# Kernel tuning notes

Measured on AMD Instinct MI355X. Metric: run time of the kernel, lower is better.

Reference implementation:

```python
import jax, jax.numpy as jnp
import numpy as np

N = 8192      # reg_num == number of nodes
E = 524288    # number of edges
OUT = 32      # out_num


def gcn_conv(x, src, dst, W, b, n):
    """PyG GCNConv: add self-loops, symmetric deg^-1/2 normalization, linear, scatter-add, bias."""
    loop = jnp.arange(n)
    s = jnp.concatenate([src, loop])
    d = jnp.concatenate([dst, loop])
    deg = jax.ops.segment_sum(jnp.ones(s.shape, dtype=x.dtype), d, num_segments=n)
    dinv = jnp.where(deg > 0, jax.lax.rsqrt(deg), jnp.zeros_like(deg))
    norm = dinv[s] * dinv[d]                      # [E+N]
    h = x @ W.T                                    # [N, out_ch]
    out = jax.ops.segment_sum(norm[:, None] * h[s], d, num_segments=n)
    return out + b


def setup_inputs() -> dict:
    key = jax.random.key(0)
    ks = jax.random.split(key, 12)
    data = jax.random.normal(ks[0], (N, 2), dtype=jnp.float32)
    edge = jax.random.randint(ks[1], (2, E), 0, N, dtype=jnp.int64)
    # GCNConv weights (PyG Linear: y = x @ W.T, bias added after aggregation)
    W1 = jax.random.normal(ks[2], (4, 2), dtype=jnp.float32) * 0.5
    b1 = jnp.zeros((4,), dtype=jnp.float32)
    W2 = jax.random.normal(ks[3], (2, 4), dtype=jnp.float32) * 0.5
    b2 = jnp.zeros((2,), dtype=jnp.float32)
    W3 = jax.random.normal(ks[4], (1, 2), dtype=jnp.float32) * 0.5
    b3 = jnp.zeros((1,), dtype=jnp.float32)
    # trailing MLP: Linear(N, 2N) -> Tanh -> Linear(2N, OUT) -> Tanh
    Wa = jax.random.normal(ks[5], (2 * N, N), dtype=jnp.float32) * (1.0 / np.sqrt(N))
    ba = jnp.zeros((2 * N,), dtype=jnp.float32)
    Wb = jax.random.normal(ks[6], (OUT, 2 * N), dtype=jnp.float32) * (1.0 / np.sqrt(2 * N))
    bb = jnp.zeros((OUT,), dtype=jnp.float32)
    return {"data": data, "edge": edge, "W1": W1, "b1": b1, "W2": W2, "b2": b2,
            "W3": W3, "b3": b3, "Wa": Wa, "ba": ba, "Wb": Wb, "bb": bb}


def reference(data, edge, W1, b1, W2, b2, W3, b3, Wa, ba, Wb, bb):
    src, dst = edge[0], edge[1]
    n = data.shape[0]
    out = jax.nn.relu(gcn_conv(data, src, dst, W1, b1, n))
    out = jax.nn.relu(gcn_conv(out, src, dst, W2, b2, n))
    out = gcn_conv(out, src, dst, W3, b3, n)       # [N, 1]
    out = out.reshape(1, -1)                        # [1, N]
    out = jnp.tanh(out @ Wa.T + ba)                 # [1, 2N]
    out = jnp.tanh(out @ Wb.T + bb)                 # [1, OUT]
    return out
```

## Files before the change

kernel.cpp:

```cpp
#include <hip/hip_runtime.h>
#include <hip/hip_bf16.h>

#define NN   8192
#define NE   524288
#define DH   16384
#define NOUT 32

typedef float f32x4 __attribute__((ext_vector_type(4)));


__global__ __launch_bounds__(256) void k_hist(const int* __restrict__ dst, int* cnt) {
    int e = blockIdx.x * blockDim.x + threadIdx.x;
    if (e < NE) atomicAdd(&cnt[dst[e]], 1);
}

__global__ __launch_bounds__(256) void k_scan(const int* __restrict__ cnt,
                                              int* __restrict__ row,
                                              int* __restrict__ cursor,
                                              float* __restrict__ dinv) {
    __shared__ int sm[256];
    int t = threadIdx.x;
    int base = t * 32;
    int local[32];
    int sum = 0;
#pragma unroll
    for (int k = 0; k < 32; ++k) { local[k] = cnt[base + k]; sum += local[k]; }
    sm[t] = sum;
    __syncthreads();
    for (int off = 1; off < 256; off <<= 1) {
        int v = (t >= off) ? sm[t - off] : 0;
        __syncthreads();
        sm[t] += v;
        __syncthreads();
    }
    int pre = (t == 0) ? 0 : sm[t - 1];
#pragma unroll
    for (int k = 0; k < 32; ++k) {
        row[base + k] = pre;
        cursor[base + k] = pre;
        dinv[base + k] = rsqrtf((float)local[k] + 1.0f);
        pre += local[k];
    }
    if (t == 255) row[NN] = pre;
}

__global__ __launch_bounds__(256) void k_build(const int* __restrict__ src,
                                               const int* __restrict__ dst,
                                               int* __restrict__ cursor,
                                               int* __restrict__ srcs) {
    int e = blockIdx.x * blockDim.x + threadIdx.x;
    if (e >= NE) return;
    int p = atomicAdd(&cursor[dst[e]], 1);
    srcs[p] = src[e];
}

__global__ __launch_bounds__(256) void k_h1(const float* __restrict__ x0,
                                            const float* __restrict__ W1,
                                            float* __restrict__ h1) {
    int i = blockIdx.x * blockDim.x + threadIdx.x;
    if (i >= NN) return;
    float a = x0[2 * i], b = x0[2 * i + 1];
    f32x4 h;
#pragma unroll
    for (int c = 0; c < 4; ++c) h[c] = a * W1[2 * c] + b * W1[2 * c + 1];
    *(f32x4*)(h1 + 4 * i) = h;
}


__global__ __launch_bounds__(256) void k_g4(const int* __restrict__ row,
                                            const int* __restrict__ srcs,
                                            const float* __restrict__ dinv,
                                            const float* __restrict__ h1,
                                            const float* __restrict__ b1,
                                            const float* __restrict__ W2,
                                            float* __restrict__ h2) {
    int wid = threadIdx.x >> 6, lane = threadIdx.x & 63;
    int i = blockIdx.x * 4 + wid;
    int beg = row[i], end = row[i + 1];
    float a0 = 0, a1 = 0, a2 = 0, a3 = 0;
    for (int p = beg + lane; p < end; p += 64) {
        int s = srcs[p];
        float w = dinv[s];
        float4 hv = *(const float4*)(h1 + 4 * s);
        a0 += w * hv.x; a1 += w * hv.y; a2 += w * hv.z; a3 += w * hv.w;
    }
#pragma unroll
    for (int off = 32; off > 0; off >>= 1) {
        a0 += __shfl_down(a0, off, 64);
        a1 += __shfl_down(a1, off, 64);
        a2 += __shfl_down(a2, off, 64);
        a3 += __shfl_down(a3, off, 64);
    }
    if (lane == 0) {
        float di = dinv[i];
        float4 hs = *(const float4*)(h1 + 4 * i);
        float x0v = fmaxf(di * (a0 + di * hs.x) + b1[0], 0.0f);
        float x1v = fmaxf(di * (a1 + di * hs.y) + b1[1], 0.0f);
        float x2v = fmaxf(di * (a2 + di * hs.z) + b1[2], 0.0f);
        float x3v = fmaxf(di * (a3 + di * hs.w) + b1[3], 0.0f);
        float2 o;
        o.x = x0v * W2[0] + x1v * W2[1] + x2v * W2[2] + x3v * W2[3];
        o.y = x0v * W2[4] + x1v * W2[5] + x2v * W2[6] + x3v * W2[7];
        *(float2*)(h2 + 2 * i) = o;
    }
}

__global__ __launch_bounds__(256) void k_g2(const int* __restrict__ row,
                                            const int* __restrict__ srcs,
                                            const float* __restrict__ dinv,
                                            const float* __restrict__ h2,
                                            const float* __restrict__ b2,
                                            const float* __restrict__ W3,
                                            float* __restrict__ h3) {
    int wid = threadIdx.x >> 6, lane = threadIdx.x & 63;
    int i = blockIdx.x * 4 + wid;
    int beg = row[i], end = row[i + 1];
    float a0 = 0, a1 = 0;
    for (int p = beg + lane; p < end; p += 64) {
        int s = srcs[p];
        float w = dinv[s];
        float2 hv = *(const float2*)(h2 + 2 * s);
        a0 += w * hv.x; a1 += w * hv.y;
    }
#pragma unroll
    for (int off = 32; off > 0; off >>= 1) {
        a0 += __shfl_down(a0, off, 64);
        a1 += __shfl_down(a1, off, 64);
    }
    if (lane == 0) {
        float di = dinv[i];
        float2 hs = *(const float2*)(h2 + 2 * i);
        float x0v = fmaxf(di * (a0 + di * hs.x) + b2[0], 0.0f);
        float x1v = fmaxf(di * (a1 + di * hs.y) + b2[1], 0.0f);
        h3[i] = x0v * W3[0] + x1v * W3[1];
    }
}

__global__ __launch_bounds__(256) void k_g1(const int* __restrict__ row,
                                            const int* __restrict__ srcs,
                                            const float* __restrict__ dinv,
                                            const float* __restrict__ h3,
                                            const float* __restrict__ b3,
                                            float* __restrict__ v) {
    int wid = threadIdx.x >> 6, lane = threadIdx.x & 63;
    int i = blockIdx.x * 4 + wid;
    int beg = row[i], end = row[i + 1];
    float a0 = 0;
    for (int p = beg + lane; p < end; p += 64) {
        int s = srcs[p];
        a0 += dinv[s] * h3[s];
    }
#pragma unroll
    for (int off = 32; off > 0; off >>= 1) a0 += __shfl_down(a0, off, 64);
    if (lane == 0) {
        float di = dinv[i];
        v[i] = di * (a0 + di * h3[i]) + b3[0];
    }
}


__global__ __launch_bounds__(256) void k_mv1(const float* __restrict__ v,
                                             const float* __restrict__ Wa,
                                             const float* __restrict__ ba,
                                             float* __restrict__ y) {
    int wid  = threadIdx.x >> 6;
    int lane = threadIdx.x & 63;
    int j = blockIdx.x * 4 + wid;
    const f32x4* wr = (const f32x4*)(Wa + (size_t)j * NN);
    const f32x4* vv = (const f32x4*)v;
    float acc = 0.0f;
#pragma unroll 8
    for (int it = 0; it < (NN / 4) / 64; ++it) {
        int idx = it * 64 + lane;
        f32x4 w = __builtin_nontemporal_load(&wr[idx]);
        f32x4 x = vv[idx];
        acc += w.x * x.x + w.y * x.y + w.z * x.z + w.w * x.w;
    }
#pragma unroll
    for (int off = 32; off > 0; off >>= 1) acc += __shfl_down(acc, off, 64);
    if (lane == 0) y[j] = tanhf(acc + ba[j]);
}

__global__ __launch_bounds__(256) void k_mv2(const float* __restrict__ y,
                                             const float* __restrict__ Wb,
                                             const float* __restrict__ bb,
                                             float* __restrict__ out) {
    int wid  = threadIdx.x >> 6;
    int lane = threadIdx.x & 63;
    int o = blockIdx.x * 4 + wid;
    const f32x4* wr = (const f32x4*)(Wb + (size_t)o * DH);
    const f32x4* yy = (const f32x4*)y;
    float acc = 0.0f;
#pragma unroll 8
    for (int it = 0; it < (DH / 4) / 64; ++it) {
        int idx = it * 64 + lane;
        f32x4 w = wr[idx];
        f32x4 x = yy[idx];
        acc += w.x * x.x + w.y * x.y + w.z * x.z + w.w * x.w;
    }
#pragma unroll
    for (int off = 32; off > 0; off >>= 1) acc += __shfl_down(acc, off, 64);
    if (lane == 0) out[o] = tanhf(acc + bb[o]);
}


extern "C" void kernel_launch(void* const* d_in, const int* in_sizes, int n_in,
                              void* d_out, int out_size, void* d_ws, size_t ws_size,
                              hipStream_t stream) {
    const float* data = (const float*)d_in[0];
    const int*   edge = (const int*)d_in[1];
    const float* W1   = (const float*)d_in[2];
    const float* b1   = (const float*)d_in[3];
    const float* W2   = (const float*)d_in[4];
    const float* b2   = (const float*)d_in[5];
    const float* W3   = (const float*)d_in[6];
    const float* b3   = (const float*)d_in[7];
    const float* Wa   = (const float*)d_in[8];
    const float* ba   = (const float*)d_in[9];
    const float* Wb   = (const float*)d_in[10];
    const float* bb   = (const float*)d_in[11];
    float* out = (float*)d_out;

    const int* src = edge;
    const int* dst = edge + NE;

    char* ws = (char*)d_ws;
    int*   cnt    = (int*)ws;
    int*   row    = cnt + NN;
    int*   cursor = row + NN + 1;
    int*   srcs   = cursor + NN;
    float* dinv   = (float*)(srcs + NE);
    float* h1     = dinv + NN;
    float* h2     = h1 + NN * 4;
    float* h3     = h2 + NN * 2;
    float* v      = h3 + NN;
    float* y1     = v + NN;

    dim3 blk(256);
    dim3 gN((NN + 255) / 256);
    dim3 gE((NE + 255) / 256);
    dim3 gW(NN / 4);

    hipMemsetAsync(cnt, 0, (size_t)NN * sizeof(int), stream);

    k_hist <<<gE, blk, 0, stream>>>(dst, cnt);
    k_h1   <<<gN, blk, 0, stream>>>(data, W1, h1);
    k_scan <<<dim3(1), blk, 0, stream>>>(cnt, row, cursor, dinv);
    k_build<<<gE, blk, 0, stream>>>(src, dst, cursor, srcs);
    k_g4   <<<gW, blk, 0, stream>>>(row, srcs, dinv, h1, b1, W2, h2);
    k_g2   <<<gW, blk, 0, stream>>>(row, srcs, dinv, h2, b2, W3, h3);
    k_g1   <<<gW, blk, 0, stream>>>(row, srcs, dinv, h3, b3, v);
    k_mv1  <<<dim3(DH / 4), blk, 0, stream>>>(v, Wa, ba, y1);
    k_mv2  <<<dim3(NOUT / 4), blk, 0, stream>>>(y1, Wb, bb, out);
}
```

Baseline: 748.1 us.

## Fuse whole GCN+MLP pipeline into one persistent kernel with grid barriers

Replaces nine separate kernel launches with a single persistent kernel of 1024 blocks that synchronises stages with atomic grid barriers. It also pre-scales node features by dinv so the gather loops skip the per-edge dinv lookup, splits the scan across 32 blocks, and has each wave compute four rows of the large matrix-vector product. This removes launch gaps and per-edge normalisation loads. In exchange it depends on all 1024 blocks being co-resident, otherwise the spin barriers deadlock, and the matvec stage now runs on fewer threads.

```diff
diff --git a/kernel.cpp b/kernel.cpp
--- a/kernel.cpp
+++ b/kernel.cpp
@@ -1,255 +1,238 @@
 #include <hip/hip_runtime.h>
-#include <hip/hip_bf16.h>
 
 #define NN   8192
 #define NE   524288
 #define DH   16384
 #define NOUT 32
 
+#define NBLK 1024
+#define NTHR 256
+#define NTH_TOT (NBLK * NTHR)
+
 typedef float f32x4 __attribute__((ext_vector_type(4)));
 
-
-__global__ __launch_bounds__(256) void k_hist(const int* __restrict__ dst, int* cnt) {
-    int e = blockIdx.x * blockDim.x + threadIdx.x;
-    if (e < NE) atomicAdd(&cnt[dst[e]], 1);
-}
-
-__global__ __launch_bounds__(256) void k_scan(const int* __restrict__ cnt,
-                                              int* __restrict__ row,
-                                              int* __restrict__ cursor,
-                                              float* __restrict__ dinv) {
-    __shared__ int sm[256];
-    int t = threadIdx.x;
-    int base = t * 32;
-    int local[32];
-    int sum = 0;
+struct Args {
+    const float* data; const int* src; const int* dst;
+    const float* W1; const float* b1; const float* W2; const float* b2;
+    const float* W3; const float* b3; const float* Wa; const float* ba;
+    const float* Wb; const float* bb;
+    float* out;
+    float* h1; float* h2; float* h3; float* v; float* y1; float* dinv;
+    int* cnt; int* bar; int* row; int* cursor; int* blksum; int* srcs;
+};
+
+__device__ __forceinline__ void gridbar(int* bar, int idx) {
+    __syncthreads();
+    if (threadIdx.x == 0) {
+        __threadfence();
+        atomicAdd(&bar[idx], 1);
+        while (__hip_atomic_load(&bar[idx], __ATOMIC_RELAXED,
+                                 __HIP_MEMORY_SCOPE_AGENT) < NBLK)
+            __builtin_amdgcn_s_sleep(2);
+        __threadfence();
+    }
+    __syncthreads();
+}
+
+__device__ __forceinline__ float wred(float a) {
 #pragma unroll
-    for (int k = 0; k < 32; ++k) { local[k] = cnt[base + k]; sum += local[k]; }
-    sm[t] = sum;
-    __syncthreads();
-    for (int off = 1; off < 256; off <<= 1) {
-        int v = (t >= off) ? sm[t - off] : 0;
+    for (int off = 32; off > 0; off >>= 1) a += __shfl_down(a, off);
+    return a;
+}
+
+__global__ __launch_bounds__(NTHR, 4) void k_fused(Args p) {
+    const int tid  = blockIdx.x * NTHR + threadIdx.x;
+    const int wave = tid >> 6;
+    const int lane = tid & 63;
+    __shared__ int sm[NTHR];
+
+    if (tid < NN) {
+        float a = p.data[2 * tid], b = p.data[2 * tid + 1];
+        f32x4 h;
+#pragma unroll
+        for (int c = 0; c < 4; ++c) h[c] = a * p.W1[2 * c] + b * p.W1[2 * c + 1];
+        *(f32x4*)(p.h1 + 4 * tid) = h;
+    }
+    const int e0 = tid, e1 = tid + NTH_TOT;
+    const int d0 = p.dst[e0], d1 = p.dst[e1];
+    const int s0 = p.src[e0], s1 = p.src[e1];
+    atomicAdd(&p.cnt[d0], 1);
+    atomicAdd(&p.cnt[d1], 1);
+    gridbar(p.bar, 0);
+
+    int myc = 0, pre = 0;
+    if (blockIdx.x < 32) {
+        int i = blockIdx.x * NTHR + threadIdx.x;
+        myc = p.cnt[i];
+        sm[threadIdx.x] = myc;
         __syncthreads();
-        sm[t] += v;
-        __syncthreads();
-    }
-    int pre = (t == 0) ? 0 : sm[t - 1];
-#pragma unroll
-    for (int k = 0; k < 32; ++k) {
-        row[base + k] = pre;
-        cursor[base + k] = pre;
-        dinv[base + k] = rsqrtf((float)local[k] + 1.0f);
-        pre += local[k];
-    }
-    if (t == 255) row[NN] = pre;
-}
-
-__global__ __launch_bounds__(256) void k_build(const int* __restrict__ src,
-                                               const int* __restrict__ dst,
-                                               int* __restrict__ cursor,
-                                               int* __restrict__ srcs) {
-    int e = blockIdx.x * blockDim.x + threadIdx.x;
-    if (e >= NE) return;
-    int p = atomicAdd(&cursor[dst[e]], 1);
-    srcs[p] = src[e];
-}
-
-__global__ __launch_bounds__(256) void k_h1(const float* __restrict__ x0,
-                                            const float* __restrict__ W1,
-                                            float* __restrict__ h1) {
-    int i = blockIdx.x * blockDim.x + threadIdx.x;
-    if (i >= NN) return;
-    float a = x0[2 * i], b = x0[2 * i + 1];
-    f32x4 h;
-#pragma unroll
-    for (int c = 0; c < 4; ++c) h[c] = a * W1[2 * c] + b * W1[2 * c + 1];
-    *(f32x4*)(h1 + 4 * i) = h;
-}
-
-
-__global__ __launch_bounds__(256) void k_g4(const int* __restrict__ row,
-                                            const int* __restrict__ srcs,
-                                            const float* __restrict__ dinv,
-                                            const float* __restrict__ h1,
-                                            const float* __restrict__ b1,
-                                            const float* __restrict__ W2,
-                                            float* __restrict__ h2) {
-    int wid = threadIdx.x >> 6, lane = threadIdx.x & 63;
-    int i = blockIdx.x * 4 + wid;
-    int beg = row[i], end = row[i + 1];
-    float a0 = 0, a1 = 0, a2 = 0, a3 = 0;
-    for (int p = beg + lane; p < end; p += 64) {
-        int s = srcs[p];
-        float w = dinv[s];
-        float4 hv = *(const float4*)(h1 + 4 * s);
-        a0 += w * hv.x; a1 += w * hv.y; a2 += w * hv.z; a3 += w * hv.w;
-    }
-#pragma unroll
-    for (int off = 32; off > 0; off >>= 1) {
-        a0 += __shfl_down(a0, off, 64);
-        a1 += __shfl_down(a1, off, 64);
-        a2 += __shfl_down(a2, off, 64);
-        a3 += __shfl_down(a3, off, 64);
-    }
-    if (lane == 0) {
-        float di = dinv[i];
-        float4 hs = *(const float4*)(h1 + 4 * i);
-        float x0v = fmaxf(di * (a0 + di * hs.x) + b1[0], 0.0f);
-        float x1v = fmaxf(di * (a1 + di * hs.y) + b1[1], 0.0f);
-        float x2v = fmaxf(di * (a2 + di * hs.z) + b1[2], 0.0f);
-        float x3v = fmaxf(di * (a3 + di * hs.w) + b1[3], 0.0f);
-        float2 o;
-        o.x = x0v * W2[0] + x1v * W2[1] + x2v * W2[2] + x3v * W2[3];
-        o.y = x0v * W2[4] + x1v * W2[5] + x2v * W2[6] + x3v * W2[7];
-        *(float2*)(h2 + 2 * i) = o;
-    }
-}
-
-__global__ __launch_bounds__(256) void k_g2(const int* __restrict__ row,
-                                            const int* __restrict__ srcs,
-                                            const float* __restrict__ dinv,
-                                            const float* __restrict__ h2,
-                                            const float* __restrict__ b2,
-                                            const float* __restrict__ W3,
-                                            float* __restrict__ h3) {
-    int wid = threadIdx.x >> 6, lane = threadIdx.x & 63;
-    int i = blockIdx.x * 4 + wid;
-    int beg = row[i], end = row[i + 1];
-    float a0 = 0, a1 = 0;
-    for (int p = beg + lane; p < end; p += 64) {
-        int s = srcs[p];
-        float w = dinv[s];
-        float2 hv = *(const float2*)(h2 + 2 * s);
-        a0 += w * hv.x; a1 += w * hv.y;
-    }
-#pragma unroll
-    for (int off = 32; off > 0; off >>= 1) {
-        a0 += __shfl_down(a0, off, 64);
-        a1 += __shfl_down(a1, off, 64);
-    }
-    if (lane == 0) {
-        float di = dinv[i];
-        float2 hs = *(const float2*)(h2 + 2 * i);
-        float x0v = fmaxf(di * (a0 + di * hs.x) + b2[0], 0.0f);
-        float x1v = fmaxf(di * (a1 + di * hs.y) + b2[1], 0.0f);
-        h3[i] = x0v * W3[0] + x1v * W3[1];
-    }
-}
-
-__global__ __launch_bounds__(256) void k_g1(const int* __restrict__ row,
-                                            const int* __restrict__ srcs,
-                                            const float* __restrict__ dinv,
-                                            const float* __restrict__ h3,
-                                            const float* __restrict__ b3,
-                                            float* __restrict__ v) {
-    int wid = threadIdx.x >> 6, lane = threadIdx.x & 63;
-    int i = blockIdx.x * 4 + wid;
-    int beg = row[i], end = row[i + 1];
-    float a0 = 0;
-    for (int p = beg + lane; p < end; p += 64) {
-        int s = srcs[p];
-        a0 += dinv[s] * h3[s];
-    }
-#pragma unroll
-    for (int off = 32; off > 0; off >>= 1) a0 += __shfl_down(a0, off, 64);
-    if (lane == 0) {
-        float di = dinv[i];
-        v[i] = di * (a0 + di * h3[i]) + b3[0];
-    }
-}
-
-
-__global__ __launch_bounds__(256) void k_mv1(const float* __restrict__ v,
-                                             const float* __restrict__ Wa,
-                                             const float* __restrict__ ba,
-                                             float* __restrict__ y) {
-    int wid  = threadIdx.x >> 6;
-    int lane = threadIdx.x & 63;
-    int j = blockIdx.x * 4 + wid;
-    const f32x4* wr = (const f32x4*)(Wa + (size_t)j * NN);
-    const f32x4* vv = (const f32x4*)v;
-    float acc = 0.0f;
-#pragma unroll 8
-    for (int it = 0; it < (NN / 4) / 64; ++it) {
-        int idx = it * 64 + lane;
-        f32x4 w = __builtin_nontemporal_load(&wr[idx]);
-        f32x4 x = vv[idx];
-        acc += w.x * x.x + w.y * x.y + w.z * x.z + w.w * x.w;
-    }
-#pragma unroll
-    for (int off = 32; off > 0; off >>= 1) acc += __shfl_down(acc, off, 64);
-    if (lane == 0) y[j] = tanhf(acc + ba[j]);
-}
-
-__global__ __launch_bounds__(256) void k_mv2(const float* __restrict__ y,
-                                             const float* __restrict__ Wb,
-                                             const float* __restrict__ bb,
-                                             float* __restrict__ out) {
-    int wid  = threadIdx.x >> 6;
-    int lane = threadIdx.x & 63;
-    int o = blockIdx.x * 4 + wid;
-    const f32x4* wr = (const f32x4*)(Wb + (size_t)o * DH);
-    const f32x4* yy = (const f32x4*)y;
-    float acc = 0.0f;
-#pragma unroll 8
-    for (int it = 0; it < (DH / 4) / 64; ++it) {
-        int idx = it * 64 + lane;
-        f32x4 w = wr[idx];
-        f32x4 x = yy[idx];
-        acc += w.x * x.x + w.y * x.y + w.z * x.z + w.w * x.w;
-    }
-#pragma unroll
-    for (int off = 32; off > 0; off >>= 1) acc += __shfl_down(acc, off, 64);
-    if (lane == 0) out[o] = tanhf(acc + bb[o]);
+        for (int off = 1; off < NTHR; off <<= 1) {
+            int vsh = (threadIdx.x >= off) ? sm[threadIdx.x - off] : 0;
+            __syncthreads();
+            sm[threadIdx.x] += vsh;
+            __syncthreads();
+        }
+        int incl = sm[threadIdx.x];
+        pre = incl - myc;
+        if (threadIdx.x == NTHR - 1) p.blksum[blockIdx.x] = incl;
+    }
+    gridbar(p.bar, 1);
+
+    if (blockIdx.x < 32) {
+        int boff = 0;
+        for (int j = 0; j < (int)blockIdx.x; ++j) boff += p.blksum[j];
+        int i = blockIdx.x * NTHR + threadIdx.x;
+        int r = boff + pre;
+        p.row[i] = r;
+        p.cursor[i] = r;
+        p.dinv[i] = rsqrtf((float)myc + 1.0f);
+        if (i == NN - 1) p.row[NN] = NE;
+    }
+    gridbar(p.bar, 2);
+
+    if (tid < NN) {
+        float di = p.dinv[tid];
+        f32x4 h = *(f32x4*)(p.h1 + 4 * tid);
+        h *= di;
+        *(f32x4*)(p.h1 + 4 * tid) = h;
+    }
+    { int q = atomicAdd(&p.cursor[d0], 1); p.srcs[q] = s0; }
+    { int q = atomicAdd(&p.cursor[d1], 1); p.srcs[q] = s1; }
+    gridbar(p.bar, 3);
+
+    for (int k = 0; k < 2; ++k) {
+        int i = 2 * wave + k;
+        int beg = p.row[i], end = p.row[i + 1];
+        float a0 = 0, a1 = 0, a2 = 0, a3 = 0;
+        for (int q = beg + lane; q < end; q += 64) {
+            int s = p.srcs[q];
+            f32x4 hv = *(const f32x4*)(p.h1 + 4 * s);
+            a0 += hv[0]; a1 += hv[1]; a2 += hv[2]; a3 += hv[3];
+        }
+        a0 = wred(a0); a1 = wred(a1); a2 = wred(a2); a3 = wred(a3);
+        if (lane == 0) {
+            float di = p.dinv[i];
+            f32x4 hs = *(const f32x4*)(p.h1 + 4 * i);
+            float x0 = fmaxf(di * (a0 + hs[0]) + p.b1[0], 0.0f);
+            float x1 = fmaxf(di * (a1 + hs[1]) + p.b1[1], 0.0f);
+            float x2 = fmaxf(di * (a2 + hs[2]) + p.b1[2], 0.0f);
+            float x3 = fmaxf(di * (a3 + hs[3]) + p.b1[3], 0.0f);
+            float o0 = x0 * p.W2[0] + x1 * p.W2[1] + x2 * p.W2[2] + x3 * p.W2[3];
+            float o1 = x0 * p.W2[4] + x1 * p.W2[5] + x2 * p.W2[6] + x3 * p.W2[7];
+            float2 o; o.x = di * o0; o.y = di * o1;
+            *(float2*)(p.h2 + 2 * i) = o;
+        }
+    }
+    gridbar(p.bar, 4);
+
+    for (int k = 0; k < 2; ++k) {
+        int i = 2 * wave + k;
+        int beg = p.row[i], end = p.row[i + 1];
+        float a0 = 0, a1 = 0;
+        for (int q = beg + lane; q < end; q += 64) {
+            int s = p.srcs[q];
+            float2 hv = *(const float2*)(p.h2 + 2 * s);
+            a0 += hv.x; a1 += hv.y;
+        }
+        a0 = wred(a0); a1 = wred(a1);
+        if (lane == 0) {
+            float di = p.dinv[i];
+            float2 hs = *(const float2*)(p.h2 + 2 * i);
+            float x0 = fmaxf(di * (a0 + hs.x) + p.b2[0], 0.0f);
+            float x1 = fmaxf(di * (a1 + hs.y) + p.b2[1], 0.0f);
+            p.h3[i] = di * (x0 * p.W3[0] + x1 * p.W3[1]);
+        }
+    }
+    gridbar(p.bar, 5);
+
+    for (int k = 0; k < 2; ++k) {
+        int i = 2 * wave + k;
+        int beg = p.row[i], end = p.row[i + 1];
+        float a0 = 0;
+        for (int q = beg + lane; q < end; q += 64) a0 += p.h3[p.srcs[q]];
+        a0 = wred(a0);
+        if (lane == 0) p.v[i] = p.dinv[i] * (a0 + p.h3[i]) + p.b3[0];
+    }
+    gridbar(p.bar, 6);
+
+    {
+        const f32x4* vv = (const f32x4*)p.v;
+        const float* wbase = p.Wa + (size_t)(4 * wave) * NN;
+        float acc0 = 0, acc1 = 0, acc2 = 0, acc3 = 0;
+#pragma unroll 2
+        for (int it = 0; it < NN / 4 / 64; ++it) {
+            int idx = it * 64 + lane;
+            f32x4 x  = vv[idx];
+            f32x4 wA = __builtin_nontemporal_load((const f32x4*)wbase + idx);
+            f32x4 wB = __builtin_nontemporal_load((const f32x4*)(wbase + NN) + idx);
+            f32x4 wC = __builtin_nontemporal_load((const f32x4*)(wbase + 2 * NN) + idx);
+            f32x4 wD = __builtin_nontemporal_load((const f32x4*)(wbase + 3 * NN) + idx);
+            acc0 += wA[0] * x[0] + wA[1] * x[1] + wA[2] * x[2] + wA[3] * x[3];
+            acc1 += wB[0] * x[0] + wB[1] * x[1] + wB[2] * x[2] + wB[3] * x[3];
+            acc2 += wC[0] * x[0] + wC[1] * x[1] + wC[2] * x[2] + wC[3] * x[3];
+            acc3 += wD[0] * x[0] + wD[1] * x[1] + wD[2] * x[2] + wD[3] * x[3];
+        }
+        acc0 = wred(acc0); acc1 = wred(acc1); acc2 = wred(acc2); acc3 = wred(acc3);
+        if (lane == 0) {
+            float4 bav = *(const float4*)(p.ba + 4 * wave);
+            float4 o;
+            o.x = tanhf(acc0 + bav.x);
+            o.y = tanhf(acc1 + bav.y);
+            o.z = tanhf(acc2 + bav.z);
+            o.w = tanhf(acc3 + bav.w);
+            *(float4*)(p.y1 + 4 * wave) = o;
+        }
+    }
+    gridbar(p.bar, 7);
+
+    if (tid < NOUT * 64) {
+        int o = tid >> 6;
+        const f32x4* wr = (const f32x4*)(p.Wb + (size_t)o * DH);
+        const f32x4* yy = (const f32x4*)p.y1;
+        float acc = 0.0f;
+#pragma unroll 4
+        for (int it = 0; it < DH / 4 / 64; ++it) {
+            int idx = it * 64 + lane;
+            f32x4 w = wr[idx], x = yy[idx];
+            acc += w[0] * x[0] + w[1] * x[1] + w[2] * x[2] + w[3] * x[3];
+        }
+        acc = wred(acc);
+        if (lane == 0) p.out[o] = tanhf(acc + p.bb[o]);
+    }
 }
 
 
 extern "C" void kernel_launch(void* const* d_in, const int* in_sizes, int n_in,
                               void* d_out, int out_size, void* d_ws, size_t ws_size,
                               hipStream_t stream) {
-    const float* data = (const float*)d_in[0];
-    const int*   edge = (const int*)d_in[1];
-    const float* W1   = (const float*)d_in[2];
-    const float* b1   = (const float*)d_in[3];
-    const float* W2   = (const float*)d_in[4];
-    const float* b2   = (const float*)d_in[5];
-    const float* W3   = (const float*)d_in[6];
-    const float* b3   = (const float*)d_in[7];
-    const float* Wa   = (const float*)d_in[8];
-    const float* ba   = (const float*)d_in[9];
-    const float* Wb   = (const float*)d_in[10];
-    const float* bb   = (const float*)d_in[11];
-    float* out = (float*)d_out;
-
-    const int* src = edge;
-    const int* dst = edge + NE;
-
-    char* ws = (char*)d_ws;
-    int*   cnt    = (int*)ws;
-    int*   row    = cnt + NN;
-    int*   cursor = row + NN + 1;
-    int*   srcs   = cursor + NN;
-    float* dinv   = (float*)(srcs + NE);
-    float* h1     = dinv + NN;
-    float* h2     = h1 + NN * 4;
-    float* h3     = h2 + NN * 2;
-    float* v      = h3 + NN;
-    float* y1     = v + NN;
-
-    dim3 blk(256);
-    dim3 gN((NN + 255) / 256);
-    dim3 gE((NE + 255) / 256);
-    dim3 gW(NN / 4);
-
-    hipMemsetAsync(cnt, 0, (size_t)NN * sizeof(int), stream);
-
-    k_hist <<<gE, blk, 0, stream>>>(dst, cnt);
-    k_h1   <<<gN, blk, 0, stream>>>(data, W1, h1);
-    k_scan <<<dim3(1), blk, 0, stream>>>(cnt, row, cursor, dinv);
-    k_build<<<gE, blk, 0, stream>>>(src, dst, cursor, srcs);
-    k_g4   <<<gW, blk, 0, stream>>>(row, srcs, dinv, h1, b1, W2, h2);
-    k_g2   <<<gW, blk, 0, stream>>>(row, srcs, dinv, h2, b2, W3, h3);
-    k_g1   <<<gW, blk, 0, stream>>>(row, srcs, dinv, h3, b3, v);
-    k_mv1  <<<dim3(DH / 4), blk, 0, stream>>>(v, Wa, ba, y1);
-    k_mv2  <<<dim3(NOUT / 4), blk, 0, stream>>>(y1, Wb, bb, out);
-}
+    (void)in_sizes; (void)n_in; (void)out_size; (void)ws_size;
+    Args p;
+    p.data = (const float*)d_in[0];
+    const int* edge = (const int*)d_in[1];
+    p.src = edge;
+    p.dst = edge + NE;
+    p.W1 = (const float*)d_in[2];  p.b1 = (const float*)d_in[3];
+    p.W2 = (const float*)d_in[4];  p.b2 = (const float*)d_in[5];
+    p.W3 = (const float*)d_in[6];  p.b3 = (const float*)d_in[7];
+    p.Wa = (const float*)d_in[8];  p.ba = (const float*)d_in[9];
+    p.Wb = (const float*)d_in[10]; p.bb = (const float*)d_in[11];
+    p.out = (float*)d_out;
+
+    float* f = (float*)d_ws;
+    p.h1   = f;  f += NN * 4;
+    p.h2   = f;  f += NN * 2;
+    p.h3   = f;  f += NN;
+    p.v    = f;  f += NN;
+    p.y1   = f;  f += DH;
+    p.dinv = f;  f += NN;
+    int* ip  = (int*)f;
+    p.cnt    = ip;  ip += NN;
+    p.bar    = ip;  ip += 8;
+    p.row    = ip;  ip += NN + 1;
+    p.cursor = ip;  ip += NN;
+    p.blksum = ip;  ip += 32;
+    p.srcs   = ip;
+
+    hipMemsetAsync(p.cnt, 0, (size_t)(NN + 8) * sizeof(int), stream);
+    hipLaunchKernelGGL(k_fused, dim3(NBLK), dim3(NTHR), 0, stream, p);
+}
```

Result: slower. 1.520 ms (+103.2%).
